# Kernel tuning notes

Measured on AMD Instinct MI355X. Metric: run time of the kernel, lower is better.

## Reference

```python
import jax, jax.numpy as jnp
import numpy as np

D_MODEL = 768
N_HEADS = 12
HEAD_DIM = D_MODEL // N_HEADS
D_FF = 4 * D_MODEL
EPS = 1e-5


def setup_inputs() -> dict:
    key = jax.random.key(0)
    ks = jax.random.split(key, 16)
    s = 0.02
    x = jax.random.normal(ks[0], (2, 2048, D_MODEL), dtype=jnp.float32)
    wq = jax.random.normal(ks[1], (D_MODEL, D_MODEL), dtype=jnp.float32) * s
    bq = jnp.zeros((D_MODEL,), jnp.float32)
    wk = jax.random.normal(ks[2], (D_MODEL, D_MODEL), dtype=jnp.float32) * s
    bk = jnp.zeros((D_MODEL,), jnp.float32)
    wv = jax.random.normal(ks[3], (D_MODEL, D_MODEL), dtype=jnp.float32) * s
    bv = jnp.zeros((D_MODEL,), jnp.float32)
    wo = jax.random.normal(ks[4], (D_MODEL, D_MODEL), dtype=jnp.float32) * s
    bo = jnp.zeros((D_MODEL,), jnp.float32)
    w1 = jax.random.normal(ks[5], (D_MODEL, D_FF), dtype=jnp.float32) * s
    b1 = jnp.zeros((D_FF,), jnp.float32)
    w2 = jax.random.normal(ks[6], (D_FF, D_MODEL), dtype=jnp.float32) * s
    b2 = jnp.zeros((D_MODEL,), jnp.float32)
    ln1_g = jnp.ones((D_MODEL,), jnp.float32)
    ln1_b = jnp.zeros((D_MODEL,), jnp.float32)
    ln2_g = jnp.ones((D_MODEL,), jnp.float32)
    ln2_b = jnp.zeros((D_MODEL,), jnp.float32)
    return dict(x=x, wq=wq, bq=bq, wk=wk, bk=bk, wv=wv, bv=bv, wo=wo, bo=bo,
                w1=w1, b1=b1, w2=w2, b2=b2,
                ln1_g=ln1_g, ln1_b=ln1_b, ln2_g=ln2_g, ln2_b=ln2_b)


def _layernorm(x, g, b):
    mu = jnp.mean(x, axis=-1, keepdims=True)
    var = jnp.mean(jnp.square(x - mu), axis=-1, keepdims=True)
    return (x - mu) * jax.lax.rsqrt(var + EPS) * g + b


def _attention(x, wq, bq, wk, bk, wv, bv, wo, bo):
    B, S, D = x.shape
    def split_heads(t):  # [B,S,D] -> [B,H,S,Hd]
        return t.reshape(B, S, N_HEADS, HEAD_DIM).transpose(0, 2, 1, 3)
    q = split_heads(x @ wq + bq)
    k = split_heads(x @ wk + bk)
    v = split_heads(x @ wv + bv)
    scores = jnp.einsum('bhqd,bhkd->bhqk', q, k) / np.sqrt(HEAD_DIM).astype(np.float32)
    causal = jnp.tril(jnp.ones((S, S), dtype=bool))
    scores = jnp.where(causal, scores, -jnp.inf)
    weights = jax.nn.softmax(scores, axis=-1)
    attn = jnp.einsum('bhqk,bhkd->bhqd', weights, v)
    attn = attn.transpose(0, 2, 1, 3).reshape(B, S, D)
    return attn @ wo + bo


def reference(x, wq, bq, wk, bk, wv, bv, wo, bo, w1, b1, w2, b2,
              ln1_g, ln1_b, ln2_g, ln2_b):
    x = x + _attention(_layernorm(x, ln1_g, ln1_b), wq, bq, wk, bk, wv, bv, wo, bo)
    h = _layernorm(x, ln2_g, ln2_b)
    ff = jax.nn.relu(h @ w1 + b1) @ w2 + b2
    return x + ff
```

## Files before the change

kernel.cpp:

```cpp
#include <hip/hip_runtime.h>
#include <stdint.h>

typedef __bf16 bf16;
typedef float f32x4 __attribute__((ext_vector_type(4)));
typedef bf16 bf16x8 __attribute__((ext_vector_type(8)));
typedef bf16 bf16x4 __attribute__((ext_vector_type(4)));

#define MFMA16(a, b, c) __builtin_amdgcn_mfma_f32_16x16x32_bf16((a), (b), (c), 0, 0, 0)

static __device__ __forceinline__ void load_lds16(const bf16* g, bf16* l) {
  __builtin_amdgcn_global_load_lds(
      (const __attribute__((address_space(1))) void*)g,
      (__attribute__((address_space(3))) void*)l, 16, 0, 0);
}

__global__ void __launch_bounds__(256) k_prep(
    const float* __restrict__ x, const float* __restrict__ ln1g,
    const float* __restrict__ ln1b, bf16* __restrict__ h1,
    const float* s0, const float* s1, const float* s2, const float* s3,
    const float* s4, const float* s5,
    bf16* d0, bf16* d1, bf16* d2, bf16* d3, bf16* d4, bf16* d5) {
  int t = blockIdx.x;
  int tid = threadIdx.x;
  if (t < 6912) {
    const float* src; bf16* dst; int R, C;
    if (t < 2304) {
      int z = t / 576; t -= z * 576;
      src = (z == 0) ? s0 : (z == 1) ? s1 : (z == 2) ? s2 : s3;
      dst = (z == 0) ? d0 : (z == 1) ? d1 : (z == 2) ? d2 : d3;
      R = 768; C = 768;
    } else if (t < 4608) {
      t -= 2304; src = s4; dst = d4; R = 768; C = 3072;
    } else {
      t -= 4608; src = s5; dst = d5; R = 3072; C = 768;
    }
    int tcn = C >> 5;
    int tr = t / tcn, tc = t % tcn;
    __shared__ float tile[32][33];
    int tx = tid & 31, ty = tid >> 5;
    for (int i = 0; i < 4; i++)
      tile[ty + i * 8][tx] = src[(size_t)(tr * 32 + ty + i * 8) * C + tc * 32 + tx];
    __syncthreads();
    for (int i = 0; i < 4; i++)
      dst[(size_t)(tc * 32 + ty + i * 8) * R + tr * 32 + tx] = (bf16)tile[tx][ty + i * 8];
  } else {
    int row = t - 6912;
    const float* rp = x + (size_t)row * 768;
    float v0 = rp[tid], v1 = rp[tid + 256], v2 = rp[tid + 512];
    float s = v0 + v1 + v2, sq = v0 * v0 + v1 * v1 + v2 * v2;
    for (int off = 1; off < 64; off <<= 1) {
      s += __shfl_xor(s, off, 64);
      sq += __shfl_xor(sq, off, 64);
    }
    __shared__ float ps[8];
    if ((tid & 63) == 0) { ps[tid >> 6] = s; ps[4 + (tid >> 6)] = sq; }
    __syncthreads();
    s = ps[0] + ps[1] + ps[2] + ps[3];
    sq = ps[4] + ps[5] + ps[6] + ps[7];
    float mu = s * (1.0f / 768.0f);
    float rstd = rsqrtf(sq * (1.0f / 768.0f) - mu * mu + 1e-5f);
    bf16* op = h1 + (size_t)row * 768;
    op[tid] = (bf16)((v0 - mu) * rstd * ln1g[tid] + ln1b[tid]);
    op[tid + 256] = (bf16)((v1 - mu) * rstd * ln1g[tid + 256] + ln1b[tid + 256]);
    op[tid + 512] = (bf16)((v2 - mu) * rstd * ln1g[tid + 512] + ln1b[tid + 512]);
  }
}

__global__ void __launch_bounds__(256) k_ln2_reduce(
    const float* __restrict__ p0, const float* __restrict__ p1,
    const float* __restrict__ x, const float* __restrict__ bo,
    const float* __restrict__ gam, const float* __restrict__ bet,
    float* __restrict__ x1, bf16* __restrict__ h2) {
  int row = blockIdx.x, tid = threadIdx.x;
  size_t base = (size_t)row * 768;
  float v0 = p0[base + tid] + p1[base + tid] + x[base + tid] + bo[tid];
  float v1 = p0[base + tid + 256] + p1[base + tid + 256] + x[base + tid + 256] + bo[tid + 256];
  float v2 = p0[base + tid + 512] + p1[base + tid + 512] + x[base + tid + 512] + bo[tid + 512];
  x1[base + tid] = v0; x1[base + tid + 256] = v1; x1[base + tid + 512] = v2;
  float s = v0 + v1 + v2, sq = v0 * v0 + v1 * v1 + v2 * v2;
  for (int off = 1; off < 64; off <<= 1) {
    s += __shfl_xor(s, off, 64);
    sq += __shfl_xor(sq, off, 64);
  }
  __shared__ float ps[8];
  if ((tid & 63) == 0) { ps[tid >> 6] = s; ps[4 + (tid >> 6)] = sq; }
  __syncthreads();
  s = ps[0] + ps[1] + ps[2] + ps[3];
  sq = ps[4] + ps[5] + ps[6] + ps[7];
  float mu = s * (1.0f / 768.0f);
  float rstd = rsqrtf(sq * (1.0f / 768.0f) - mu * mu + 1e-5f);
  bf16* op = h2 + base;
  op[tid] = (bf16)((v0 - mu) * rstd * gam[tid] + bet[tid]);
  op[tid + 256] = (bf16)((v1 - mu) * rstd * gam[tid + 256] + bet[tid + 256]);
  op[tid + 512] = (bf16)((v2 - mu) * rstd * gam[tid + 512] + bet[tid + 512]);
}

__global__ void __launch_bounds__(256) k_ff2_reduce(
    const float* __restrict__ f0, const float* __restrict__ f1,
    const float* __restrict__ f2, const float* __restrict__ f3,
    const float* __restrict__ x1, const float* __restrict__ b2,
    float* __restrict__ out) {
  size_t i = ((size_t)blockIdx.x * 256 + threadIdx.x) * 4;
  int col = (int)(i % 768);
  f32x4 v = *(const f32x4*)(x1 + i);
  f32x4 b = *(const f32x4*)(b2 + col);
  f32x4 a0 = *(const f32x4*)(f0 + i), a1 = *(const f32x4*)(f1 + i);
  f32x4 a2 = *(const f32x4*)(f2 + i), a3 = *(const f32x4*)(f3 + i);
  *(f32x4*)(out + i) = v + b + a0 + a1 + a2 + a3;
}

template <int MT>
static __device__ __forceinline__ void gemm_core(
    const bf16* __restrict__ A, int lda, const bf16* __restrict__ Bt, int ldb,
    int Kc, int m0, int n0, bf16* As, bf16* Bs, f32x4 acc[MT][4]) {
  int tid = threadIdx.x, w = tid >> 6, lane = tid & 63, quad = lane >> 4, l15 = lane & 15;
  int wr = w >> 1, wc = w & 1;
  int srow = lane >> 2, sk = (lane & 3) * 8;
  const int ABUF = MT * 32 * 32;
  const int BBUF = 128 * 32;

  auto stage = [&](int k0, int buf) {
    bf16* Ab = As + buf * ABUF;
    bf16* Bb = Bs + buf * BBUF;
    if (MT == 4) {
      for (int c = 0; c < 2; c++) {
        int seg = w * 2 + c;
        load_lds16(A + (size_t)(m0 + seg * 16 + srow) * lda + k0 + sk, Ab + seg * 512);
      }
    } else {
      load_lds16(A + (size_t)(m0 + w * 16 + srow) * lda + k0 + sk, Ab + w * 512);
    }
    for (int c = 0; c < 2; c++) {
      int seg = w * 2 + c;
      load_lds16(Bt + (size_t)(n0 + seg * 16 + srow) * ldb + k0 + sk, Bb + seg * 512);
    }
  };

  stage(0, 0);
  int cur = 0;
  for (int k0 = 0; k0 < Kc; k0 += 32) {
    __syncthreads();
    if (k0 + 32 < Kc) stage(k0 + 32, cur ^ 1);
    const bf16* Ab = As + cur * ABUF;
    const bf16* Bb = Bs + cur * BBUF;
    bf16x8 af[MT], bfr[4];
    for (int mi = 0; mi < MT; mi++)
      af[mi] = *(const bf16x8*)(Ab + (wr * (MT * 16) + mi * 16 + l15) * 32 + quad * 8);
    for (int ni = 0; ni < 4; ni++)
      bfr[ni] = *(const bf16x8*)(Bb + (wc * 64 + ni * 16 + l15) * 32 + quad * 8);
    for (int mi = 0; mi < MT; mi++)
      for (int ni = 0; ni < 4; ni++)
        acc[mi][ni] = MFMA16(af[mi], bfr[ni], acc[mi][ni]);
    cur ^= 1;
  }
}

template <int MT>
__global__ void __launch_bounds__(256, 3) k_gemm(
    const bf16* __restrict__ A, const bf16* __restrict__ Bt,
    const float* __restrict__ bias, bf16* __restrict__ outp, int K_, int N_) {
  __shared__ __align__(16) bf16 As[2 * MT * 32 * 32];
  __shared__ __align__(16) bf16 Bs[2 * 128 * 32];
  int m0 = blockIdx.y * (MT * 32), n0 = blockIdx.x * 128;
  f32x4 acc[MT][4] = {};
  gemm_core<MT>(A, K_, Bt, K_, K_, m0, n0, As, Bs, acc);
  int tid = threadIdx.x, w = tid >> 6, lane = tid & 63, quad = lane >> 4, l15 = lane & 15;
  int wr = w >> 1, wc = w & 1;
  float bv[4];
  for (int ni = 0; ni < 4; ni++) bv[ni] = bias[n0 + wc * 64 + ni * 16 + l15];
  for (int mi = 0; mi < MT; mi++) {
    int mb = m0 + wr * (MT * 16) + mi * 16 + quad * 4;
    for (int ni = 0; ni < 4; ni++) {
      int n = n0 + wc * 64 + ni * 16 + l15;
      for (int r = 0; r < 4; r++) {
        float val = acc[mi][ni][r] + bv[ni];
        outp[(size_t)(mb + r) * N_ + n] = (bf16)fmaxf(val, 0.0f);
      }
    }
  }
}

template <int MT>
__global__ void __launch_bounds__(256, 3) k_gemm_split(
    const bf16* __restrict__ A, const bf16* __restrict__ Bt,
    float* __restrict__ f0, float* __restrict__ f1,
    float* __restrict__ f2, float* __restrict__ f3, int K_, int Kc, int N_) {
  __shared__ __align__(16) bf16 As[2 * MT * 32 * 32];
  __shared__ __align__(16) bf16 Bs[2 * 128 * 32];
  int z = blockIdx.z;
  float* outp = (z == 0) ? f0 : (z == 1) ? f1 : (z == 2) ? f2 : f3;
  int m0 = blockIdx.y * (MT * 32), n0 = blockIdx.x * 128;
  f32x4 acc[MT][4] = {};
  gemm_core<MT>(A + (size_t)z * Kc, K_, Bt + (size_t)z * Kc, K_, Kc, m0, n0, As, Bs, acc);
  int tid = threadIdx.x, w = tid >> 6, lane = tid & 63, quad = lane >> 4, l15 = lane & 15;
  int wr = w >> 1, wc = w & 1;
  for (int mi = 0; mi < MT; mi++) {
    int mb = m0 + wr * (MT * 16) + mi * 16 + quad * 4;
    for (int ni = 0; ni < 4; ni++) {
      int n = n0 + wc * 64 + ni * 16 + l15;
      for (int r = 0; r < 4; r++)
        outp[(size_t)(mb + r) * N_ + n] = acc[mi][ni][r];
    }
  }
}

template <int MT>
__global__ void __launch_bounds__(256, 3) k_gemm_qkv(
    const bf16* __restrict__ h1, const bf16* __restrict__ wqT,
    const bf16* __restrict__ wkT, const bf16* __restrict__ wvT,
    const float* __restrict__ bq, const float* __restrict__ bk,
    const float* __restrict__ bv, bf16* __restrict__ qb,
    bf16* __restrict__ kb, bf16* __restrict__ vtb) {
  __shared__ __align__(16) bf16 As[2 * MT * 32 * 32];
  __shared__ __align__(16) bf16 Bs[2 * 128 * 32];
  int z = blockIdx.z;
  const bf16* Bt = (z == 0) ? wqT : (z == 1) ? wkT : wvT;
  const float* bias = (z == 0) ? bq : (z == 1) ? bk : bv;
  int m0 = blockIdx.y * (MT * 32), n0 = blockIdx.x * 128;
  f32x4 acc[MT][4] = {};
  gemm_core<MT>(h1, 768, Bt, 768, 768, m0, n0, As, Bs, acc);
  int tid = threadIdx.x, w = tid >> 6, lane = tid & 63, quad = lane >> 4, l15 = lane & 15;
  int wr = w >> 1, wc = w & 1;
  float bvv[4];
  for (int ni = 0; ni < 4; ni++) bvv[ni] = bias[n0 + wc * 64 + ni * 16 + l15];
  for (int mi = 0; mi < MT; mi++) {
    int mb = m0 + wr * (MT * 16) + mi * 16 + quad * 4;
    int b = mb >> 11, s0_ = mb & 2047;
    for (int ni = 0; ni < 4; ni++) {
      int n = n0 + wc * 64 + ni * 16 + l15;
      int h = n >> 6, hd = n & 63;
      if (z < 2) {
        bf16* outp = (z == 0) ? qb : kb;
        size_t base = (size_t)(b * 12 + h) * 2048 * 64;
        for (int r = 0; r < 4; r++)
          outp[base + (size_t)(s0_ + r) * 64 + hd] = (bf16)(acc[mi][ni][r] + bvv[ni]);
      } else {
        bf16x4 pk;
        for (int r = 0; r < 4; r++) pk[r] = (bf16)(acc[mi][ni][r] + bvv[ni]);
        *(bf16x4*)(vtb + (((size_t)(b * 12 + h) * 64 + hd) * 2048 + s0_)) = pk;
      }
    }
  }
}

__global__ void __launch_bounds__(256, 2) k_attn(
    const bf16* __restrict__ qb, const bf16* __restrict__ kb,
    const bf16* __restrict__ vtb, bf16* __restrict__ out) {
  __shared__ __align__(16) bf16 Ks[2 * 128 * 64];
  __shared__ __align__(16) bf16 Vs[2 * 64 * 128];
  __shared__ __align__(16) bf16 Ps[4][16 * 128];
  int qt = 31 - (blockIdx.x / 24);
  int bh = blockIdx.x % 24;
  int q0 = qt * 64;
  int tid = threadIdx.x, w = tid >> 6, lane = tid & 63, quad = lane >> 4, l15 = lane & 15;
  const bf16* qbase = qb + (size_t)bh * 2048 * 64;
  const bf16* kbase = kb + (size_t)bh * 2048 * 64;
  const bf16* vbase = vtb + (size_t)bh * 64 * 2048;

  bf16x8 qf[2];
  for (int ds = 0; ds < 2; ds++)
    qf[ds] = *(const bf16x8*)(qbase + (size_t)(q0 + w * 16 + l15) * 64 + ds * 32 + quad * 8);

  bf16 one_ = (bf16)1.0f;
  bf16x8 ones8 = {one_, one_, one_, one_, one_, one_, one_, one_};

  f32x4 o[4] = {};
  f32x4 lacc = {};

  auto stageKV = [&](int k0, int buf) {
    int rsub = lane >> 3, c8 = lane & 7;
    bf16* Kb = Ks + buf * (128 * 64);
    for (int c = 0; c < 4; c++) {
      int seg = c * 4 + w;
      int row = seg * 8 + rsub;
      load_lds16(kbase + (size_t)(k0 + row) * 64 + ((c8 ^ (row & 7)) * 8), Kb + seg * 512);
    }
    int rsub2 = lane >> 4, c16 = lane & 15;
    bf16* Vb = Vs + buf * (64 * 128);
    for (int c = 0; c < 4; c++) {
      int seg = c * 4 + w;
      int row = seg * 4 + rsub2;
      load_lds16(vbase + (size_t)row * 2048 + k0 + ((c16 ^ (row & 15)) * 8), Vb + seg * 512);
    }
  };

  const float C2 = 0.18033688011112042f;
  int nkt = (qt >> 1) + 1;
  stageKV(0, 0);
  int cur = 0;
  for (int kt = 0; kt < nkt; kt++) {
    int k0 = kt * 128;
    __syncthreads();
    if (kt + 1 < nkt) stageKV(k0 + 128, cur ^ 1);
    const bf16* Kb = Ks + cur * (128 * 64);
    const bf16* Vb = Vs + cur * (64 * 128);

    f32x4 sc[8] = {};
    __builtin_amdgcn_s_setprio(1);
    for (int kj = 0; kj < 8; kj++) {
      int krow = kj * 16 + l15;
      for (int ds = 0; ds < 2; ds++) {
        bf16x8 kf = *(const bf16x8*)(Kb + krow * 64 + (((ds * 4 + quad) ^ (krow & 7)) * 8));
        sc[kj] = MFMA16(qf[ds], kf, sc[kj]);
      }
    }
    __builtin_amdgcn_s_setprio(0);
    if (kt == nkt - 1) {
      int qg = q0 + w * 16 + quad * 4;
      for (int kj = 0; kj < 8; kj++) {
        int kg = k0 + kj * 16 + l15;
        for (int r = 0; r < 4; r++)
          if (kg > qg + r) sc[kj][r] = -3.0e38f;
      }
    }
    for (int kj = 0; kj < 8; kj++)
      for (int r = 0; r < 4; r++)
        sc[kj][r] = exp2f(sc[kj][r] * C2);
    for (int kj = 0; kj < 8; kj++) {
      int colb = kj * 16 + l15;
      int chb = colb >> 3, cin = colb & 7;
      for (int r = 0; r < 4; r++) {
        int prow = quad * 4 + r;
        Ps[w][prow * 128 + ((chb ^ prow) * 8) + cin] = (bf16)sc[kj][r];
      }
    }
    __builtin_amdgcn_s_setprio(1);
    for (int ks = 0; ks < 4; ks++) {
      int prow = l15;
      bf16x8 pf = *(const bf16x8*)(&Ps[w][prow * 128 + (((ks * 4 + quad) ^ prow) * 8)]);
      lacc = MFMA16(pf, ones8, lacc);
      for (int dj = 0; dj < 4; dj++) {
        int vrow = dj * 16 + l15;
        bf16x8 vf = *(const bf16x8*)(Vb + vrow * 128 + (((ks * 4 + quad) ^ (vrow & 15)) * 8));
        o[dj] = MFMA16(pf, vf, o[dj]);
      }
    }
    __builtin_amdgcn_s_setprio(0);
    cur ^= 1;
  }
  int b = bh / 12, h = bh % 12;
  f32x4 rl;
  for (int r = 0; r < 4; r++) rl[r] = 1.0f / lacc[r];
  int srow = q0 + w * 16 + quad * 4;
  for (int dj = 0; dj < 4; dj++) {
    int d = h * 64 + dj * 16 + l15;
    for (int r = 0; r < 4; r++)
      out[(size_t)(b * 2048 + srow + r) * 768 + d] = (bf16)(o[dj][r] * rl[r]);
  }
}

extern "C" void kernel_launch(void* const* d_in, const int* in_sizes, int n_in,
                              void* d_out, int out_size, void* d_ws, size_t ws_size,
                              hipStream_t stream) {
  const float* x    = (const float*)d_in[0];
  const float* wq   = (const float*)d_in[1];
  const float* bq   = (const float*)d_in[2];
  const float* wk   = (const float*)d_in[3];
  const float* bk   = (const float*)d_in[4];
  const float* wv   = (const float*)d_in[5];
  const float* bv   = (const float*)d_in[6];
  const float* wo   = (const float*)d_in[7];
  const float* bo   = (const float*)d_in[8];
  const float* w1   = (const float*)d_in[9];
  const float* b1   = (const float*)d_in[10];
  const float* w2   = (const float*)d_in[11];
  const float* b2   = (const float*)d_in[12];
  const float* ln1g = (const float*)d_in[13];
  const float* ln1b = (const float*)d_in[14];
  const float* ln2g = (const float*)d_in[15];
  const float* ln2b = (const float*)d_in[16];

  char* p = (char*)d_ws;
  bf16* wqT = (bf16*)p; p += (size_t)768 * 768 * 2;
  bf16* wkT = (bf16*)p; p += (size_t)768 * 768 * 2;
  bf16* wvT = (bf16*)p; p += (size_t)768 * 768 * 2;
  bf16* woT = (bf16*)p; p += (size_t)768 * 768 * 2;
  bf16* w1T = (bf16*)p; p += (size_t)768 * 3072 * 2;
  bf16* w2T = (bf16*)p; p += (size_t)768 * 3072 * 2;
  bf16* h1   = (bf16*)p; p += (size_t)4096 * 768 * 2;
  bf16* qbuf = (bf16*)p; p += (size_t)4096 * 768 * 2;
  bf16* kbuf = (bf16*)p; p += (size_t)4096 * 768 * 2;
  bf16* vtb  = (bf16*)p; p += (size_t)4096 * 768 * 2;
  bf16* att  = (bf16*)p; p += (size_t)4096 * 768 * 2;
  float* x1  = (float*)p; p += (size_t)4096 * 768 * 4;
  bf16* h2   = (bf16*)p; p += (size_t)4096 * 768 * 2;
  bf16* ffm  = (bf16*)p; p += (size_t)4096 * 3072 * 2;
  float* p0  = (float*)p; p += (size_t)4096 * 768 * 4;
  float* p1  = (float*)p; p += (size_t)4096 * 768 * 4;
  float* f0 = (float*)h1;
  float* f1 = (float*)kbuf;
  float* f2 = p0;
  float* f3 = p1;

  k_prep<<<dim3(11008), dim3(256), 0, stream>>>(
      x, ln1g, ln1b, h1, wq, wk, wv, wo, w1, w2, wqT, wkT, wvT, woT, w1T, w2T);
  k_gemm_qkv<4><<<dim3(6, 32, 3), dim3(256), 0, stream>>>(
      h1, wqT, wkT, wvT, bq, bk, bv, qbuf, kbuf, vtb);
  k_attn<<<dim3(768), dim3(256), 0, stream>>>(qbuf, kbuf, vtb, att);
  k_gemm_split<2><<<dim3(6, 64, 2), dim3(256), 0, stream>>>(
      att, woT, p0, p1, p0, p1, 768, 384, 768);
  k_ln2_reduce<<<dim3(4096), dim3(256), 0, stream>>>(
      p0, p1, x, bo, ln2g, ln2b, x1, h2);
  k_gemm<4><<<dim3(24, 32), dim3(256), 0, stream>>>(
      h2, w1T, b1, ffm, 768, 3072);
  k_gemm_split<4><<<dim3(6, 32, 4), dim3(256), 0, stream>>>(
      ffm, w2T, f0, f1, f2, f3, 3072, 768, 768);
  k_ff2_reduce<<<dim3(3072), dim3(256), 0, stream>>>(
      f0, f1, f2, f3, x1, b2, (float*)d_out);
}
```

Before: 279.2 us.

## Replace split-K partial buffers and reduce kernels with atomic accumulation into residual

The split-K GEMMs for the output projection and FF2 now atomically add their partial sums straight into buffers pre-initialised with the residual plus bias. x1 is seeded with x+bo in the prep kernel and out is seeded with x1+b2 in the LN2 kernel. This removes the separate ff2 reduce kernel and the fp32 partial-buffer traffic. It also switches the QKV GEMM to a smaller M tile. Atomics make the fp32 summation order nondeterministic and add atomic memory traffic in the epilogues.

```diff
diff --git a/kernel.cpp b/kernel.cpp
--- a/kernel.cpp
+++ b/kernel.cpp
@@ -17,6 +17,7 @@
 __global__ void __launch_bounds__(256) k_prep(
     const float* __restrict__ x, const float* __restrict__ ln1g,
     const float* __restrict__ ln1b, bf16* __restrict__ h1,
+    const float* __restrict__ bo, float* __restrict__ x1,
     const float* s0, const float* s1, const float* s2, const float* s3,
     const float* s4, const float* s5,
     bf16* d0, bf16* d1, bf16* d2, bf16* d3, bf16* d4, bf16* d5) {
@@ -43,7 +44,7 @@
     __syncthreads();
     for (int i = 0; i < 4; i++)
       dst[(size_t)(tc * 32 + ty + i * 8) * R + tr * 32 + tx] = (bf16)tile[tx][ty + i * 8];
-  } else {
+  } else if (t < 11008) {
     int row = t - 6912;
     const float* rp = x + (size_t)row * 768;
     float v0 = rp[tid], v1 = rp[tid + 256], v2 = rp[tid + 512];
@@ -63,20 +64,25 @@
     op[tid] = (bf16)((v0 - mu) * rstd * ln1g[tid] + ln1b[tid]);
     op[tid + 256] = (bf16)((v1 - mu) * rstd * ln1g[tid + 256] + ln1b[tid + 256]);
     op[tid + 512] = (bf16)((v2 - mu) * rstd * ln1g[tid + 512] + ln1b[tid + 512]);
-  }
-}
-
-__global__ void __launch_bounds__(256) k_ln2_reduce(
-    const float* __restrict__ p0, const float* __restrict__ p1,
-    const float* __restrict__ x, const float* __restrict__ bo,
-    const float* __restrict__ gam, const float* __restrict__ bet,
-    float* __restrict__ x1, bf16* __restrict__ h2) {
+  } else {
+    size_t i = ((size_t)(t - 11008) * 256 + tid) * 4;
+    int col = (int)(i % 768);
+    f32x4 v = *(const f32x4*)(x + i);
+    f32x4 b = *(const f32x4*)(bo + col);
+    *(f32x4*)(x1 + i) = v + b;
+  }
+}
+
+__global__ void __launch_bounds__(256) k_ln2(
+    const float* __restrict__ x1, const float* __restrict__ gam,
+    const float* __restrict__ bet, const float* __restrict__ b2,
+    bf16* __restrict__ h2, float* __restrict__ outp) {
   int row = blockIdx.x, tid = threadIdx.x;
   size_t base = (size_t)row * 768;
-  float v0 = p0[base + tid] + p1[base + tid] + x[base + tid] + bo[tid];
-  float v1 = p0[base + tid + 256] + p1[base + tid + 256] + x[base + tid + 256] + bo[tid + 256];
-  float v2 = p0[base + tid + 512] + p1[base + tid + 512] + x[base + tid + 512] + bo[tid + 512];
-  x1[base + tid] = v0; x1[base + tid + 256] = v1; x1[base + tid + 512] = v2;
+  float v0 = x1[base + tid], v1 = x1[base + tid + 256], v2 = x1[base + tid + 512];
+  outp[base + tid] = v0 + b2[tid];
+  outp[base + tid + 256] = v1 + b2[tid + 256];
+  outp[base + tid + 512] = v2 + b2[tid + 512];
   float s = v0 + v1 + v2, sq = v0 * v0 + v1 * v1 + v2 * v2;
   for (int off = 1; off < 64; off <<= 1) {
     s += __shfl_xor(s, off, 64);
@@ -93,20 +99,6 @@
   op[tid] = (bf16)((v0 - mu) * rstd * gam[tid] + bet[tid]);
   op[tid + 256] = (bf16)((v1 - mu) * rstd * gam[tid + 256] + bet[tid + 256]);
   op[tid + 512] = (bf16)((v2 - mu) * rstd * gam[tid + 512] + bet[tid + 512]);
-}
-
-__global__ void __launch_bounds__(256) k_ff2_reduce(
-    const float* __restrict__ f0, const float* __restrict__ f1,
-    const float* __restrict__ f2, const float* __restrict__ f3,
-    const float* __restrict__ x1, const float* __restrict__ b2,
-    float* __restrict__ out) {
-  size_t i = ((size_t)blockIdx.x * 256 + threadIdx.x) * 4;
-  int col = (int)(i % 768);
-  f32x4 v = *(const f32x4*)(x1 + i);
-  f32x4 b = *(const f32x4*)(b2 + col);
-  f32x4 a0 = *(const f32x4*)(f0 + i), a1 = *(const f32x4*)(f1 + i);
-  f32x4 a2 = *(const f32x4*)(f2 + i), a3 = *(const f32x4*)(f3 + i);
-  *(f32x4*)(out + i) = v + b + a0 + a1 + a2 + a3;
 }
 
 template <int MT>
@@ -181,14 +173,12 @@
 }
 
 template <int MT>
-__global__ void __launch_bounds__(256, 3) k_gemm_split(
+__global__ void __launch_bounds__(256, 3) k_gemm_split_at(
     const bf16* __restrict__ A, const bf16* __restrict__ Bt,
-    float* __restrict__ f0, float* __restrict__ f1,
-    float* __restrict__ f2, float* __restrict__ f3, int K_, int Kc, int N_) {
+    float* __restrict__ outp, int K_, int Kc, int N_) {
   __shared__ __align__(16) bf16 As[2 * MT * 32 * 32];
   __shared__ __align__(16) bf16 Bs[2 * 128 * 32];
   int z = blockIdx.z;
-  float* outp = (z == 0) ? f0 : (z == 1) ? f1 : (z == 2) ? f2 : f3;
   int m0 = blockIdx.y * (MT * 32), n0 = blockIdx.x * 128;
   f32x4 acc[MT][4] = {};
   gemm_core<MT>(A + (size_t)z * Kc, K_, Bt + (size_t)z * Kc, K_, Kc, m0, n0, As, Bs, acc);
@@ -199,7 +189,7 @@
     for (int ni = 0; ni < 4; ni++) {
       int n = n0 + wc * 64 + ni * 16 + l15;
       for (int r = 0; r < 4; r++)
-        outp[(size_t)(mb + r) * N_ + n] = acc[mi][ni][r];
+        unsafeAtomicAdd(&outp[(size_t)(mb + r) * N_ + n], acc[mi][ni][r]);
     }
   }
 }
@@ -385,26 +375,21 @@
   float* x1  = (float*)p; p += (size_t)4096 * 768 * 4;
   bf16* h2   = (bf16*)p; p += (size_t)4096 * 768 * 2;
   bf16* ffm  = (bf16*)p; p += (size_t)4096 * 3072 * 2;
-  float* p0  = (float*)p; p += (size_t)4096 * 768 * 4;
-  float* p1  = (float*)p; p += (size_t)4096 * 768 * 4;
-  float* f0 = (float*)h1;
-  float* f1 = (float*)kbuf;
-  float* f2 = p0;
-  float* f3 = p1;
-
-  k_prep<<<dim3(11008), dim3(256), 0, stream>>>(
-      x, ln1g, ln1b, h1, wq, wk, wv, wo, w1, w2, wqT, wkT, wvT, woT, w1T, w2T);
-  k_gemm_qkv<4><<<dim3(6, 32, 3), dim3(256), 0, stream>>>(
+
+  float* out = (float*)d_out;
+
+  k_prep<<<dim3(14080), dim3(256), 0, stream>>>(
+      x, ln1g, ln1b, h1, bo, x1,
+      wq, wk, wv, wo, w1, w2, wqT, wkT, wvT, woT, w1T, w2T);
+  k_gemm_qkv<2><<<dim3(6, 64, 3), dim3(256), 0, stream>>>(
       h1, wqT, wkT, wvT, bq, bk, bv, qbuf, kbuf, vtb);
   k_attn<<<dim3(768), dim3(256), 0, stream>>>(qbuf, kbuf, vtb, att);
-  k_gemm_split<2><<<dim3(6, 64, 2), dim3(256), 0, stream>>>(
-      att, woT, p0, p1, p0, p1, 768, 384, 768);
-  k_ln2_reduce<<<dim3(4096), dim3(256), 0, stream>>>(
-      p0, p1, x, bo, ln2g, ln2b, x1, h2);
+  k_gemm_split_at<2><<<dim3(6, 64, 2), dim3(256), 0, stream>>>(
+      att, woT, x1, 768, 384, 768);
+  k_ln2<<<dim3(4096), dim3(256), 0, stream>>>(
+      x1, ln2g, ln2b, b2, h2, out);
   k_gemm<4><<<dim3(24, 32), dim3(256), 0, stream>>>(
       h2, w1T, b1, ffm, 768, 3072);
-  k_gemm_split<4><<<dim3(6, 32, 4), dim3(256), 0, stream>>>(
-      ffm, w2T, f0, f1, f2, f3, 3072, 768, 768);
-  k_ff2_reduce<<<dim3(3072), dim3(256), 0, stream>>>(
-      f0, f1, f2, f3, x1, b2, (float*)d_out);
-}
+  k_gemm_split_at<4><<<dim3(6, 32, 4), dim3(256), 0, stream>>>(
+      ffm, w2T, out, 3072, 768, 768);
+}
```

Result: slower. 310.6 us (+11.3%).
